# Performance work log

Hardware: AMD Instinct MI355X
Metric: run time of the kernel (lower is better)

Reference implementation:

```python
import jax, jax.numpy as jnp
import numpy as np

B, T, C = 1, 4096, 768
H, D = 12, 64  # n_heads, head_dim

def setup_inputs() -> dict:
    key = jax.random.key(0)
    k1, k2, k3 = jax.random.split(key, 3)
    x = jax.random.normal(k1, (B, T, C), dtype=jnp.float32)
    W_qkv = jax.random.normal(k2, (3 * C, C), dtype=jnp.float32) * 0.02
    W_out = jax.random.normal(k3, (C, C), dtype=jnp.float32) * 0.02
    return {"x": x, "W_qkv": W_qkv, "W_out": W_out}

def reference(x, W_qkv, W_out):
    Bb, Tt, Cc = x.shape
    qkv = x @ W_qkv.T                      # [B,T,3C] (torch Linear: y = x W^T)
    q, k, v = jnp.split(qkv, 3, axis=-1)
    def heads(t):
        return t.reshape(Bb, Tt, H, D).transpose(0, 2, 1, 3)  # [B,H,T,D]
    q, k, v = heads(q), heads(k), heads(v)
    scale = 1.0 / np.sqrt(D).astype(np.float32)
    scores = jnp.einsum('bhqd,bhkd->bhqk', q, k) * scale       # [B,H,T,T]
    causal = jnp.triu(jnp.ones((Tt, Tt), dtype=bool), k=1)
    scores = jnp.where(causal, -jnp.inf, scores)
    weights = jax.nn.softmax(scores, axis=-1)
    out = jnp.einsum('bhqk,bhkd->bhqd', weights, v)            # [B,H,T,D]
    out = out.transpose(0, 2, 1, 3).reshape(Bb, Tt, Cc)
    return out @ W_out.T
```

## Files before the change

### kernel.cpp

```cpp
#include <hip/hip_runtime.h>
#include <math.h>

typedef __bf16 bf16x8 __attribute__((ext_vector_type(8)));
typedef __bf16 bf16x2 __attribute__((ext_vector_type(2)));
typedef float f32x4 __attribute__((ext_vector_type(4)));
typedef float f32x16 __attribute__((ext_vector_type(16)));
typedef unsigned int u32x2 __attribute__((ext_vector_type(2)));

static constexpr int TSEQ = 4096;
static constexpr int CDIM = 768;
static constexpr int NHEAD = 12;
static constexpr int HDIM = 64;
static constexpr int QKVW = 2304;

__device__ inline unsigned short f32_to_bf16(float f) {
    unsigned int u = __builtin_bit_cast(unsigned int, f);
    u = (u + 0x7FFFu + ((u >> 16) & 1u)) >> 16;
    return (unsigned short)u;
}

__device__ inline f32x4 mfma16(bf16x8 a, bf16x8 b, f32x4 c) {
    return __builtin_amdgcn_mfma_f32_16x16x32_bf16(a, b, c, 0, 0, 0);
}

__device__ inline f32x16 mfma32(bf16x8 a, bf16x8 b, f32x16 c) {
    return __builtin_amdgcn_mfma_f32_32x32x16_bf16(a, b, c, 0, 0, 0);
}

__device__ inline void pls32(unsigned int &a, unsigned int &b) {
    u32x2 r = __builtin_amdgcn_permlane32_swap(a, b, false, false);
    a = r[0];
    b = r[1];
}

__device__ inline float swap_fmax(float x) {
    unsigned int a = __builtin_bit_cast(unsigned int, x), b = a;
    pls32(a, b);
    return fmaxf(__builtin_bit_cast(float, a), __builtin_bit_cast(float, b));
}

__device__ inline float swap_fadd(float x) {
    unsigned int a = __builtin_bit_cast(unsigned int, x), b = a;
    pls32(a, b);
    return __builtin_bit_cast(float, a) + __builtin_bit_cast(float, b);
}

__device__ inline unsigned int pkbf(float a, float b) {
    bf16x2 t;
    t[0] = (__bf16)a;
    t[1] = (__bf16)b;
    return __builtin_bit_cast(unsigned int, t);
}

#define GLOAD_LDS16(g, s)                                                        \
    __builtin_amdgcn_global_load_lds(                                            \
        (const __attribute__((address_space(1))) void*)(g),                      \
        (__attribute__((address_space(3))) void*)(s), 16, 0, 0)

__global__ __launch_bounds__(256) void cvt_f32_bf16(
    const float* __restrict__ in, unsigned short* __restrict__ out, int n)
{
    int i = (blockIdx.x * 256 + threadIdx.x) * 4;
    if (i >= n) return;
    float4 v = *reinterpret_cast<const float4*>(&in[i]);
    ushort4 o;
    o.x = f32_to_bf16(v.x); o.y = f32_to_bf16(v.y);
    o.z = f32_to_bf16(v.z); o.w = f32_to_bf16(v.w);
    *reinterpret_cast<ushort4*>(&out[i]) = o;
}

template <int OUT_BF16>
__global__ __launch_bounds__(256) void gemm_nt_mfma(
    const unsigned short* __restrict__ A, const unsigned short* __restrict__ B,
    void* __restrict__ Cv, int M, int N, int K, int scale_cols, float scale)
{
    __shared__ unsigned short As[128][32];
    __shared__ unsigned short Bs[128][32];

    const int tid = threadIdx.x;
    const int w = tid >> 6, l = tid & 63;
    const int l16 = l & 15, lg = l >> 4;
    const int wy = w >> 1, wx = w & 1;
    const int m0 = blockIdx.y * 128, n0 = blockIdx.x * 128;
    const float cs = (n0 < scale_cols) ? scale : 1.0f;

    f32x4 acc[4][4];
#pragma unroll
    for (int i = 0; i < 4; ++i)
#pragma unroll
        for (int j = 0; j < 4; ++j) {
            f32x4 z = {0.f, 0.f, 0.f, 0.f};
            acc[i][j] = z;
        }

    const int lrow = l >> 2;
    const int lkb = (l & 3) * 8;

    for (int k0 = 0; k0 < K; k0 += 32) {
        __syncthreads();
#pragma unroll
        for (int p = 0; p < 2; ++p) {
            int c = w * 2 + p;
            const unsigned short* ga = &A[(size_t)(m0 + c * 16 + lrow) * K + k0 + lkb];
            GLOAD_LDS16(ga, &As[c * 16][0]);
            const unsigned short* gb = &B[(size_t)(n0 + c * 16 + lrow) * K + k0 + lkb];
            GLOAD_LDS16(gb, &Bs[c * 16][0]);
        }
        __syncthreads();

        bf16x8 af[4], bf[4];
#pragma unroll
        for (int i = 0; i < 4; ++i) {
            af[i] = *reinterpret_cast<const bf16x8*>(&As[wy * 64 + i * 16 + l16][lg * 8]);
            bf[i] = *reinterpret_cast<const bf16x8*>(&Bs[wx * 64 + i * 16 + l16][lg * 8]);
        }
#pragma unroll
        for (int i = 0; i < 4; ++i)
#pragma unroll
            for (int j = 0; j < 4; ++j)
                acc[i][j] = mfma16(af[i], bf[j], acc[i][j]);
    }

#pragma unroll
    for (int i = 0; i < 4; ++i)
#pragma unroll
        for (int j = 0; j < 4; ++j)
#pragma unroll
            for (int r = 0; r < 4; ++r) {
                int row = m0 + wy * 64 + i * 16 + lg * 4 + r;
                int col = n0 + wx * 64 + j * 16 + l16;
                float v = acc[i][j][r] * cs;
                if (OUT_BF16)
                    ((unsigned short*)Cv)[(size_t)row * N + col] = f32_to_bf16(v);
                else
                    ((float*)Cv)[(size_t)row * N + col] = v;
            }
}

__global__ __launch_bounds__(256) void transpose_v(
    const unsigned short* __restrict__ qkv, unsigned short* __restrict__ vt)
{
    __shared__ unsigned short tile[64][72];
    const int t0 = blockIdx.x * 64;
    const int c0 = blockIdx.y * 64;
    const int tid = threadIdx.x;

#pragma unroll
    for (int p = 0; p < 2; ++p) {
        int idx = tid + p * 256;
        int r = idx >> 3, ch = idx & 7;
        uint4 v = *reinterpret_cast<const uint4*>(
            &qkv[(size_t)(t0 + r) * QKVW + 1536 + c0 + ch * 8]);
        *reinterpret_cast<uint4*>(&tile[r][ch * 8]) = v;
    }
    __syncthreads();
#pragma unroll
    for (int p = 0; p < 2; ++p) {
        int idx = tid + p * 256;
        int r = idx >> 3, ch = idx & 7;
        ushort4 o[2];
#pragma unroll
        for (int j = 0; j < 8; ++j)
            ((unsigned short*)o)[j] = tile[ch * 8 + j][r];
        *reinterpret_cast<uint4*>(&vt[(size_t)(c0 + r) * TSEQ + t0 + ch * 8]) =
            *reinterpret_cast<uint4*>(o);
    }
}

__global__ __launch_bounds__(256, 3) void attn_mfma(
    const unsigned short* __restrict__ qkv,
    const unsigned short* __restrict__ vtg,
    unsigned short* __restrict__ att)
{
    __shared__ unsigned short Ks[2][64 * 64];
    __shared__ unsigned short Vs[2][64 * 64];
    __shared__ float Ms[2][64], Ls[2][64];

    const int b = blockIdx.x;
    const int h = b % NHEAD;
    const int qt = (TSEQ / 64 - 1) - b / NHEAD;
    const int q0 = qt * 64;
    const int tid = threadIdx.x;
    const int w = tid >> 6, l = tid & 63;
    const int qs = w >> 1;
    const int wk = w & 1;
    const int l32 = l & 31, hh = l >> 5;

    const int NT = qt + 1;
    const int NH = NT >> 1;
    const int ITER = NT - NH;
    const int tbase = wk ? NH : 0;
    const int tcnt  = wk ? ITER : NH;

    bf16x8 qf[4];
    {
        const unsigned short* qrow =
            &qkv[(size_t)(q0 + qs * 32 + l32) * QKVW + h * HDIM + hh * 8];
#pragma unroll
        for (int ks = 0; ks < 4; ++ks)
            qf[ks] = *reinterpret_cast<const bf16x8*>(qrow + ks * 16);
    }

    f32x16 oacc0, oacc1;
#pragma unroll
    for (int i = 0; i < 16; ++i) { oacc0[i] = 0.f; oacc1[i] = 0.f; }
    float m_s = -1e30f, l_s = 0.f;

    f32x16 zf;
#pragma unroll
    for (int i = 0; i < 16; ++i) zf[i] = 0.f;

    const int cx = l32 & 7;
    const unsigned short* kb8[4];
    const unsigned short* vb8[4];
#pragma unroll
    for (int ks = 0; ks < 4; ++ks) {
        const int sw = l32 * 64 + (((2 * ks + hh) ^ cx) * 8);
        kb8[ks] = &Ks[wk][sw];
        vb8[ks] = &Vs[wk][sw];
    }

    auto stageK = [&](int kt) {
#pragma unroll
        for (int i = 0; i < 4; ++i) {
            int u = i * 128 + qs * 64 + l;
            int r = u >> 3;
            int sc = (u & 7) ^ (r & 7);
            const unsigned short* g =
                &qkv[(size_t)(kt * 64 + r) * QKVW + CDIM + h * HDIM + sc * 8];
            GLOAD_LDS16(g, &Ks[wk][(i * 128 + qs * 64) * 8]);
        }
    };

    auto stageV = [&](int kt) {
#pragma unroll
        for (int i = 0; i < 4; ++i) {
            int u = i * 128 + qs * 64 + l;
            int r = u >> 3;
            int sc = (u & 7) ^ (r & 7);
            const unsigned short* g =
                &vtg[(size_t)(h * HDIM + r) * TSEQ + kt * 64 + sc * 8];
            GLOAD_LDS16(g, &Vs[wk][(i * 128 + qs * 64) * 8]);
        }
    };

    if (tcnt > 0) stageK(tbase);

    for (int it = 0; it < ITER; ++it) {
        const bool act = it < tcnt;
        const int kt = tbase + it;

        __syncthreads();

        if (act) stageV(kt);

        f32x16 s0, s1;
        if (act) {
            __builtin_amdgcn_s_setprio(1);
            {
                bf16x8 k0 = *reinterpret_cast<const bf16x8*>(kb8[0]);
                bf16x8 k1 = *reinterpret_cast<const bf16x8*>(kb8[0] + 2048);
                s0 = mfma32(k0, qf[0], zf);
                s1 = mfma32(k1, qf[0], zf);
            }
#pragma unroll
            for (int ks = 1; ks < 4; ++ks) {
                bf16x8 k0 = *reinterpret_cast<const bf16x8*>(kb8[ks]);
                bf16x8 k1 = *reinterpret_cast<const bf16x8*>(kb8[ks] + 2048);
                s0 = mfma32(k0, qf[ks], s0);
                s1 = mfma32(k1, qf[ks], s1);
            }
            __builtin_amdgcn_s_setprio(0);

            if (kt == qt) {
                const int qq = qs * 32 + l32;
#pragma unroll
                for (int rr = 0; rr < 16; ++rr) {
                    int kv0 = (rr & 3) + 8 * (rr >> 2) + 4 * hh;
                    if (kv0 > qq) s0[rr] = -1e30f;
                    if (kv0 + 32 > qq) s1[rr] = -1e30f;
                }
            }

            float ma = fmaxf(fmaxf(s0[0], s0[1]), s0[2]);
            float mb = fmaxf(fmaxf(s0[3], s0[4]), s0[5]);
            float mc = fmaxf(fmaxf(s0[6], s0[7]), s0[8]);
            float md = fmaxf(fmaxf(s0[9], s0[10]), s0[11]);
            float me = fmaxf(fmaxf(s0[12], s0[13]), s0[14]);
            float mf = fmaxf(fmaxf(s0[15], s1[0]), s1[1]);
            float mg = fmaxf(fmaxf(s1[2], s1[3]), s1[4]);
            float mh = fmaxf(fmaxf(s1[5], s1[6]), s1[7]);
            float mi = fmaxf(fmaxf(s1[8], s1[9]), s1[10]);
            float mj = fmaxf(fmaxf(s1[11], s1[12]), s1[13]);
            float mk = fmaxf(s1[14], s1[15]);
            ma = fmaxf(fmaxf(ma, mb), mc);
            md = fmaxf(fmaxf(md, me), mf);
            mg = fmaxf(fmaxf(mg, mh), mi);
            mj = fmaxf(mj, mk);
            float mx = fmaxf(fmaxf(ma, md), fmaxf(mg, mj));
            mx = swap_fmax(mx);

            if (!__all(mx <= m_s + 8.0f)) {
                float mnew = fmaxf(m_s, mx);
                float alpha = exp2f(m_s - mnew);
                m_s = mnew;
                l_s *= alpha;
#pragma unroll
                for (int i = 0; i < 16; ++i) {
                    oacc0[i] *= alpha;
                    oacc1[i] *= alpha;
                }
            }

#pragma unroll
            for (int i = 0; i < 16; ++i) {
                s0[i] = exp2f(s0[i] - m_s);
                s1[i] = exp2f(s1[i] - m_s);
            }
            float ts = 0.f;
#pragma unroll
            for (int i = 0; i < 16; ++i) ts += s0[i] + s1[i];
            l_s += swap_fadd(ts);
        }

        __syncthreads();

        if (it + 1 < tcnt) stageK(tbase + it + 1);

        if (act) {
            bf16x8 pb[4];
#pragma unroll
            for (int ks = 0; ks < 4; ++ks) {
                const int r0 = (ks & 1) * 8;
                unsigned int w0, w1, w2, w3;
                if (ks < 2) {
                    w0 = pkbf(s0[r0 + 0], s0[r0 + 1]);
                    w1 = pkbf(s0[r0 + 2], s0[r0 + 3]);
                    w2 = pkbf(s0[r0 + 4], s0[r0 + 5]);
                    w3 = pkbf(s0[r0 + 6], s0[r0 + 7]);
                } else {
                    w0 = pkbf(s1[r0 + 0], s1[r0 + 1]);
                    w1 = pkbf(s1[r0 + 2], s1[r0 + 3]);
                    w2 = pkbf(s1[r0 + 4], s1[r0 + 5]);
                    w3 = pkbf(s1[r0 + 6], s1[r0 + 7]);
                }
                pls32(w0, w2);
                pls32(w1, w3);
                uint4 uv = make_uint4(w0, w1, w2, w3);
                pb[ks] = __builtin_bit_cast(bf16x8, uv);
            }

            __builtin_amdgcn_s_setprio(1);
#pragma unroll
            for (int ks = 0; ks < 4; ++ks) {
                bf16x8 v0 = *reinterpret_cast<const bf16x8*>(vb8[ks]);
                bf16x8 v1 = *reinterpret_cast<const bf16x8*>(vb8[ks] + 2048);
                oacc0 = mfma32(v0, pb[ks], oacc0);
                oacc1 = mfma32(v1, pb[ks], oacc1);
            }
            __builtin_amdgcn_s_setprio(0);
        }
    }

    __syncthreads();
    float* fb = reinterpret_cast<float*>(&Ks[0][0]) + qs * 2048;
    if (wk == 1) {
#pragma unroll
        for (int rr = 0; rr < 16; ++rr) {
            fb[rr * 64 + l] = oacc0[rr];
            fb[(16 + rr) * 64 + l] = oacc1[rr];
        }
        Ms[qs][l] = m_s;
        Ls[qs][l] = l_s;
    }
    __syncthreads();
    if (wk == 0) {
        float m1 = Ms[qs][l], l1 = Ls[qs][l];
        float mstar = fmaxf(m_s, m1);
        float a0 = exp2f(m_s - mstar), a1 = exp2f(m1 - mstar);
        float inv = 1.0f / (l_s * a0 + l1 * a1);
        a0 *= inv;
        a1 *= inv;

        unsigned short* ob = &Vs[0][0] + qs * 2304;
#pragma unroll
        for (int rr = 0; rr < 16; ++rr) {
            int d0 = (rr & 3) + 8 * (rr >> 2) + 4 * hh;
            float v0 = oacc0[rr] * a0 + fb[rr * 64 + l] * a1;
            float v1 = oacc1[rr] * a0 + fb[(16 + rr) * 64 + l] * a1;
            ob[l32 * 72 + d0] = f32_to_bf16(v0);
            ob[l32 * 72 + 32 + d0] = f32_to_bf16(v1);
        }
#pragma unroll
        for (int p = 0; p < 4; ++p) {
            int r = p * 8 + (l >> 3), c = (l & 7) * 8;
            uint4 v = *reinterpret_cast<const uint4*>(&ob[r * 72 + c]);
            *reinterpret_cast<uint4*>(
                &att[(size_t)(q0 + qs * 32 + r) * CDIM + h * HDIM + c]) = v;
        }
    }
}

extern "C" void kernel_launch(void* const* d_in, const int* in_sizes, int n_in,
                              void* d_out, int out_size, void* d_ws, size_t ws_size,
                              hipStream_t stream) {
    const float* x     = (const float*)d_in[0];
    const float* W_qkv = (const float*)d_in[1];
    const float* W_out = (const float*)d_in[2];
    float* out = (float*)d_out;

    char* ws = (char*)d_ws;
    unsigned short* xb    = (unsigned short*)(ws);
    unsigned short* wqkvb = (unsigned short*)(ws + 6291456);
    unsigned short* woutb = (unsigned short*)(ws + 9830400);
    unsigned short* qkvb  = (unsigned short*)(ws + 11010048);
    unsigned short* vtb   = (unsigned short*)(ws + 29884416);
    unsigned short* attb  = (unsigned short*)(ws + 36175872);

    cvt_f32_bf16<<<3072, 256, 0, stream>>>(x, xb, TSEQ * CDIM);
    cvt_f32_bf16<<<1728, 256, 0, stream>>>(W_qkv, wqkvb, QKVW * CDIM);
    cvt_f32_bf16<<<576, 256, 0, stream>>>(W_out, woutb, CDIM * CDIM);

    gemm_nt_mfma<1><<<dim3(QKVW / 128, TSEQ / 128), 256, 0, stream>>>(
        xb, wqkvb, qkvb, TSEQ, QKVW, CDIM, CDIM, 0.125f * 1.44269504f);

    transpose_v<<<dim3(TSEQ / 64, NHEAD), 256, 0, stream>>>(qkvb, vtb);

    attn_mfma<<<dim3(NHEAD * (TSEQ / 64)), 256, 0, stream>>>(qkvb, vtb, attb);

    gemm_nt_mfma<0><<<dim3(CDIM / 128, TSEQ / 128), 256, 0, stream>>>(
        attb, woutb, out, TSEQ, CDIM, CDIM, 0, 1.0f);
}
```

Baseline: 129.2 us.

## Split attention KV range four ways per block with 512-thread blocks

The attention kernel now runs 512 threads per block, with each of two query sub-tiles processed by four waves that each take a quarter of the causal KV tiles instead of half. The partial outputs, maxima and sums from three waves are written to shared memory and merged by the first wave using a four-way log-sum-exp combine. The aim is more parallelism per query tile and shorter serial KV loops, especially for the long causal rows. The cost is a larger shared-memory footprint, a heavier final reduction and fewer resident blocks per CU.

```diff
diff --git a/kernel.cpp b/kernel.cpp
--- a/kernel.cpp
+++ b/kernel.cpp
@@ -167,14 +167,13 @@
     }
 }
 
-__global__ __launch_bounds__(256, 3) void attn_mfma(
+__global__ __launch_bounds__(512, 2) void attn_mfma(
     const unsigned short* __restrict__ qkv,
     const unsigned short* __restrict__ vtg,
     unsigned short* __restrict__ att)
 {
-    __shared__ unsigned short Ks[2][64 * 64];
-    __shared__ unsigned short Vs[2][64 * 64];
-    __shared__ float Ms[2][64], Ls[2][64];
+    __shared__ unsigned short smem[8 * 4096];
+    __shared__ float Ms[2][4][32], Ls[2][4][32];
 
     const int b = blockIdx.x;
     const int h = b % NHEAD;
@@ -182,15 +181,14 @@
     const int q0 = qt * 64;
     const int tid = threadIdx.x;
     const int w = tid >> 6, l = tid & 63;
-    const int qs = w >> 1;
-    const int wk = w & 1;
+    const int qs = w >> 2;
+    const int wq = w & 3;
     const int l32 = l & 31, hh = l >> 5;
 
     const int NT = qt + 1;
-    const int NH = NT >> 1;
-    const int ITER = NT - NH;
-    const int tbase = wk ? NH : 0;
-    const int tcnt  = wk ? ITER : NH;
+    const int tbase = (NT * wq) >> 2;
+    const int tcnt  = ((NT * (wq + 1)) >> 2) - tbase;
+    const int ITER  = (NT + 3) >> 2;
 
     bf16x8 qf[4];
     {
@@ -216,8 +214,8 @@
 #pragma unroll
     for (int ks = 0; ks < 4; ++ks) {
         const int sw = l32 * 64 + (((2 * ks + hh) ^ cx) * 8);
-        kb8[ks] = &Ks[wk][sw];
-        vb8[ks] = &Vs[wk][sw];
+        kb8[ks] = &smem[wq * 4096 + sw];
+        vb8[ks] = &smem[16384 + wq * 4096 + sw];
     }
 
     auto stageK = [&](int kt) {
@@ -228,7 +226,7 @@
             int sc = (u & 7) ^ (r & 7);
             const unsigned short* g =
                 &qkv[(size_t)(kt * 64 + r) * QKVW + CDIM + h * HDIM + sc * 8];
-            GLOAD_LDS16(g, &Ks[wk][(i * 128 + qs * 64) * 8]);
+            GLOAD_LDS16(g, &smem[wq * 4096 + (i * 128 + qs * 64) * 8]);
         }
     };
 
@@ -240,7 +238,7 @@
             int sc = (u & 7) ^ (r & 7);
             const unsigned short* g =
                 &vtg[(size_t)(h * HDIM + r) * TSEQ + kt * 64 + sc * 8];
-            GLOAD_LDS16(g, &Vs[wk][(i * 128 + qs * 64) * 8]);
+            GLOAD_LDS16(g, &smem[16384 + wq * 4096 + (i * 128 + qs * 64) * 8]);
         }
     };
 
@@ -363,33 +361,41 @@
     }
 
     __syncthreads();
-    float* fb = reinterpret_cast<float*>(&Ks[0][0]) + qs * 2048;
-    if (wk == 1) {
+    float* fb = reinterpret_cast<float*>(&smem[0]);
+    if (wq != 0) {
+        const int slot = qs * 3 + (wq - 1);
 #pragma unroll
         for (int rr = 0; rr < 16; ++rr) {
-            fb[rr * 64 + l] = oacc0[rr];
-            fb[(16 + rr) * 64 + l] = oacc1[rr];
-        }
-        Ms[qs][l] = m_s;
-        Ls[qs][l] = l_s;
+            int d = (rr & 3) + 8 * (rr >> 2) + 4 * hh;
+            fb[slot * 2048 + d * 32 + l32] = oacc0[rr];
+            fb[slot * 2048 + (d + 32) * 32 + l32] = oacc1[rr];
+        }
+        if (hh == 0) { Ms[qs][wq][l32] = m_s; Ls[qs][wq][l32] = l_s; }
     }
     __syncthreads();
-    if (wk == 0) {
-        float m1 = Ms[qs][l], l1 = Ls[qs][l];
-        float mstar = fmaxf(m_s, m1);
+    if (wq == 0) {
+        float m1 = Ms[qs][1][l32], m2 = Ms[qs][2][l32], m3 = Ms[qs][3][l32];
+        float l1 = Ls[qs][1][l32], l2 = Ls[qs][2][l32], l3 = Ls[qs][3][l32];
+        float mstar = fmaxf(fmaxf(m_s, m1), fmaxf(m2, m3));
         float a0 = exp2f(m_s - mstar), a1 = exp2f(m1 - mstar);
-        float inv = 1.0f / (l_s * a0 + l1 * a1);
-        a0 *= inv;
-        a1 *= inv;
-
-        unsigned short* ob = &Vs[0][0] + qs * 2304;
+        float a2 = exp2f(m2 - mstar), a3 = exp2f(m3 - mstar);
+        float inv = 1.0f / (l_s * a0 + l1 * a1 + l2 * a2 + l3 * a3);
+        a0 *= inv; a1 *= inv; a2 *= inv; a3 *= inv;
+
+        const int fs = qs * 3;
+        unsigned short* ob = &smem[24576 + qs * 2304];
 #pragma unroll
         for (int rr = 0; rr < 16; ++rr) {
-            int d0 = (rr & 3) + 8 * (rr >> 2) + 4 * hh;
-            float v0 = oacc0[rr] * a0 + fb[rr * 64 + l] * a1;
-            float v1 = oacc1[rr] * a0 + fb[(16 + rr) * 64 + l] * a1;
-            ob[l32 * 72 + d0] = f32_to_bf16(v0);
-            ob[l32 * 72 + 32 + d0] = f32_to_bf16(v1);
+            int d = (rr & 3) + 8 * (rr >> 2) + 4 * hh;
+            float v0 = oacc0[rr] * a0 + fb[fs * 2048 + d * 32 + l32] * a1
+                     + fb[(fs + 1) * 2048 + d * 32 + l32] * a2
+                     + fb[(fs + 2) * 2048 + d * 32 + l32] * a3;
+            int d2 = d + 32;
+            float v1 = oacc1[rr] * a0 + fb[fs * 2048 + d2 * 32 + l32] * a1
+                     + fb[(fs + 1) * 2048 + d2 * 32 + l32] * a2
+                     + fb[(fs + 2) * 2048 + d2 * 32 + l32] * a3;
+            ob[l32 * 72 + d] = f32_to_bf16(v0);
+            ob[l32 * 72 + d2] = f32_to_bf16(v1);
         }
 #pragma unroll
         for (int p = 0; p < 4; ++p) {
@@ -426,7 +432,7 @@
 
     transpose_v<<<dim3(TSEQ / 64, NHEAD), 256, 0, stream>>>(qkvb, vtb);
 
-    attn_mfma<<<dim3(NHEAD * (TSEQ / 64)), 256, 0, stream>>>(qkvb, vtb, attb);
+    attn_mfma<<<dim3(NHEAD * (TSEQ / 64)), 512, 0, stream>>>(qkvb, vtb, attb);
 
     gemm_nt_mfma<0><<<dim3(CDIM / 128, TSEQ / 128), 256, 0, stream>>>(
         attb, woutb, out, TSEQ, CDIM, CDIM, 0, 1.0f);
```

Measured after the change: 144.9 us. 1.12x slower.

## Fuse V transpose into QKV GEMM epilogue and merge conversion kernels

Applied to the files above, without the earlier changes.

Replaces the three fp32-to-bf16 conversion launches with one kernel that handles all three buffers by index range. The QKV GEMM now writes the V column blocks straight into the transposed V buffer through an LDS staging tile, which removes the separate transpose kernel and its reread of V. This cuts launch count and memory traffic. In exchange, the QKV GEMM's LDS footprint grows by about 34KB, which may reduce occupancy, and V is no longer written into the qkv buffer.

```diff
diff --git a/kernel.cpp b/kernel.cpp
--- a/kernel.cpp
+++ b/kernel.cpp
@@ -57,25 +57,39 @@
         (const __attribute__((address_space(1))) void*)(g),                      \
         (__attribute__((address_space(3))) void*)(s), 16, 0, 0)
 
-__global__ __launch_bounds__(256) void cvt_f32_bf16(
-    const float* __restrict__ in, unsigned short* __restrict__ out, int n)
+__global__ __launch_bounds__(256) void cvt3_f32_bf16(
+    const float* __restrict__ a, int na, unsigned short* __restrict__ oa,
+    const float* __restrict__ b, int nb, unsigned short* __restrict__ ob,
+    const float* __restrict__ c, int nc, unsigned short* __restrict__ oc)
 {
     int i = (blockIdx.x * 256 + threadIdx.x) * 4;
-    if (i >= n) return;
-    float4 v = *reinterpret_cast<const float4*>(&in[i]);
+    const float* src;
+    unsigned short* dst;
+    if (i < na) {
+        src = a + i; dst = oa + i;
+    } else if ((i - na) < nb) {
+        src = b + (i - na); dst = ob + (i - na);
+    } else if ((i - na - nb) < nc) {
+        src = c + (i - na - nb); dst = oc + (i - na - nb);
+    } else {
+        return;
+    }
+    float4 v = *reinterpret_cast<const float4*>(src);
     ushort4 o;
     o.x = f32_to_bf16(v.x); o.y = f32_to_bf16(v.y);
     o.z = f32_to_bf16(v.z); o.w = f32_to_bf16(v.w);
-    *reinterpret_cast<ushort4*>(&out[i]) = o;
-}
-
-template <int OUT_BF16>
+    *reinterpret_cast<ushort4*>(dst) = o;
+}
+
+template <int OUT_BF16, int VT>
 __global__ __launch_bounds__(256) void gemm_nt_mfma(
     const unsigned short* __restrict__ A, const unsigned short* __restrict__ B,
-    void* __restrict__ Cv, int M, int N, int K, int scale_cols, float scale)
+    void* __restrict__ Cv, int M, int N, int K, int scale_cols, float scale,
+    unsigned short* __restrict__ vt)
 {
     __shared__ unsigned short As[128][32];
     __shared__ unsigned short Bs[128][32];
+    __shared__ unsigned short Ts[VT ? 128 * 136 : 1];
 
     const int tid = threadIdx.x;
     const int w = tid >> 6, l = tid & 63;
@@ -119,6 +133,30 @@
 #pragma unroll
             for (int j = 0; j < 4; ++j)
                 acc[i][j] = mfma16(af[i], bf[j], acc[i][j]);
+    }
+
+    if (VT && n0 >= 1536) {
+#pragma unroll
+        for (int i = 0; i < 4; ++i)
+#pragma unroll
+            for (int j = 0; j < 4; ++j)
+#pragma unroll
+                for (int r = 0; r < 4; ++r) {
+                    int rr = wy * 64 + i * 16 + lg * 4 + r;
+                    int cc = wx * 64 + j * 16 + l16;
+                    Ts[cc * 136 + rr] = f32_to_bf16(acc[i][j][r]);
+                }
+        __syncthreads();
+#pragma unroll
+        for (int p = 0; p < 8; ++p) {
+            int idx = p * 256 + tid;
+            int row = idx >> 4;
+            int ch = idx & 15;
+            uint4 v = *reinterpret_cast<const uint4*>(&Ts[row * 136 + ch * 8]);
+            *reinterpret_cast<uint4*>(
+                &vt[(size_t)(n0 - 1536 + row) * TSEQ + m0 + ch * 8]) = v;
+        }
+        return;
     }
 
 #pragma unroll
@@ -135,36 +173,6 @@
                 else
                     ((float*)Cv)[(size_t)row * N + col] = v;
             }
-}
-
-__global__ __launch_bounds__(256) void transpose_v(
-    const unsigned short* __restrict__ qkv, unsigned short* __restrict__ vt)
-{
-    __shared__ unsigned short tile[64][72];
-    const int t0 = blockIdx.x * 64;
-    const int c0 = blockIdx.y * 64;
-    const int tid = threadIdx.x;
-
-#pragma unroll
-    for (int p = 0; p < 2; ++p) {
-        int idx = tid + p * 256;
-        int r = idx >> 3, ch = idx & 7;
-        uint4 v = *reinterpret_cast<const uint4*>(
-            &qkv[(size_t)(t0 + r) * QKVW + 1536 + c0 + ch * 8]);
-        *reinterpret_cast<uint4*>(&tile[r][ch * 8]) = v;
-    }
-    __syncthreads();
-#pragma unroll
-    for (int p = 0; p < 2; ++p) {
-        int idx = tid + p * 256;
-        int r = idx >> 3, ch = idx & 7;
-        ushort4 o[2];
-#pragma unroll
-        for (int j = 0; j < 8; ++j)
-            ((unsigned short*)o)[j] = tile[ch * 8 + j][r];
-        *reinterpret_cast<uint4*>(&vt[(size_t)(c0 + r) * TSEQ + t0 + ch * 8]) =
-            *reinterpret_cast<uint4*>(o);
-    }
 }
 
 __global__ __launch_bounds__(256, 3) void attn_mfma(
@@ -417,17 +425,16 @@
     unsigned short* vtb   = (unsigned short*)(ws + 29884416);
     unsigned short* attb  = (unsigned short*)(ws + 36175872);
 
-    cvt_f32_bf16<<<3072, 256, 0, stream>>>(x, xb, TSEQ * CDIM);
-    cvt_f32_bf16<<<1728, 256, 0, stream>>>(W_qkv, wqkvb, QKVW * CDIM);
-    cvt_f32_bf16<<<576, 256, 0, stream>>>(W_out, woutb, CDIM * CDIM);
-
-    gemm_nt_mfma<1><<<dim3(QKVW / 128, TSEQ / 128), 256, 0, stream>>>(
-        xb, wqkvb, qkvb, TSEQ, QKVW, CDIM, CDIM, 0.125f * 1.44269504f);
-
-    transpose_v<<<dim3(TSEQ / 64, NHEAD), 256, 0, stream>>>(qkvb, vtb);
+    cvt3_f32_bf16<<<5376, 256, 0, stream>>>(
+        x, TSEQ * CDIM, xb,
+        W_qkv, QKVW * CDIM, wqkvb,
+        W_out, CDIM * CDIM, woutb);
+
+    gemm_nt_mfma<1, 1><<<dim3(QKVW / 128, TSEQ / 128), 256, 0, stream>>>(
+        xb, wqkvb, qkvb, TSEQ, QKVW, CDIM, CDIM, 0.125f * 1.44269504f, vtb);
 
     attn_mfma<<<dim3(NHEAD * (TSEQ / 64)), 256, 0, stream>>>(qkvb, vtb, attb);
 
-    gemm_nt_mfma<0><<<dim3(CDIM / 128, TSEQ / 128), 256, 0, stream>>>(
-        attb, woutb, out, TSEQ, CDIM, CDIM, 0, 1.0f);
-}
+    gemm_nt_mfma<0, 0><<<dim3(CDIM / 128, TSEQ / 128), 256, 0, stream>>>(
+        attb, woutb, out, TSEQ, CDIM, CDIM, 0, 1.0f, nullptr);
+}
```

Measured after the change: 122.6 us. 5.2% less time.
